# Kernel tuning notes

Hardware: AMD Instinct MI355X
Metric: run time of the kernel (lower is better)

The kernel has to match this reference:

```python
import jax, jax.numpy as jnp
import numpy as np

D_K = 64


def setup_inputs() -> dict:
    key = jax.random.key(0)
    kq, kk, kv, km = jax.random.split(key, 4)
    B, H, S = 4, 16, 2048
    Q = jax.random.normal(kq, (B, H, S, D_K), dtype=jnp.float32)
    K = jax.random.normal(kk, (B, H, S, D_K), dtype=jnp.float32)
    V = jax.random.normal(kv, (B, H, S, D_K), dtype=jnp.float32)
    # boolean mask, True = masked out; broadcast over heads
    mask = jax.random.randint(km, (B, 1, S, S), 0, 2).astype(jnp.bool_)
    return {"Q": Q, "K": K, "V": V, "mask": mask}


def reference(Q, K, V, mask):
    scale = jnp.sqrt(jnp.asarray(D_K, dtype=Q.dtype))
    # [B,H,S,S] scores
    scores = jnp.einsum('bhqd,bhkd->bhqk', Q, K) / scale
    scores = jnp.where(mask, jnp.asarray(-1e9, dtype=scores.dtype), scores)
    attn = jax.nn.softmax(scores, axis=-1)
    return jnp.einsum('bhqk,bhkd->bhqd', attn, V)
```

## Files before the change

kernel.cpp:

```cpp
#include <hip/hip_runtime.h>
#include <hip/hip_bf16.h>


#define SEQ   2048
#define DK    64
#define NB_   4
#define NBH   64
#define KVB   64
#define QB    128

#define MASKH_WORDS ((size_t)NB_ * SEQ * 64)

typedef float    f32x16 __attribute__((ext_vector_type(16)));
typedef _Float16 f16x8  __attribute__((ext_vector_type(8)));

#define QSCALE 0.18033688011112042f
#define MBIAS  (-5.0f)
#define CH     264

#if __has_builtin(__builtin_amdgcn_exp2f)
#define EXP2F(x) __builtin_amdgcn_exp2f(x)
#else
#define EXP2F(x) exp2f(x)
#endif

__device__ __forceinline__ unsigned pkrtz(float lo, float hi) {
  auto v = __builtin_amdgcn_cvt_pkrtz(lo, hi);
  return __builtin_bit_cast(unsigned, v);
}

#define BARRIER()                                          \
  do {                                                     \
    asm volatile("s_waitcnt lgkmcnt(0)" ::: "memory");     \
    __builtin_amdgcn_s_barrier();                          \
  } while (0)

__device__ __forceinline__ void halfswap(unsigned a, unsigned b,
                                         unsigned& out_lo, unsigned& out_hi, int hiL) {
#if __has_builtin(__builtin_amdgcn_permlane32_swap)
  auto r = __builtin_amdgcn_permlane32_swap(a, b, false, false);
  out_lo = r[0];
  out_hi = r[1];
#else
  unsigned ax = __shfl_xor(a, 32), bx = __shfl_xor(b, 32);
  out_lo = hiL ? bx : a;
  out_hi = hiL ? b : ax;
#endif
}

__global__ __launch_bounds__(256) void mask_pack2(const int* __restrict__ M,
                                                  unsigned* __restrict__ P) {
  int t  = blockIdx.x * 256 + threadIdx.x;
  int hi = t & 1, T = (t >> 1) & 31, q = (t >> 6) & 2047, b = t >> 17;
  const int* src = M + ((size_t)b * SEQ + q) * SEQ + T * 64 + 4 * hi;
  unsigned bits = 0;
#pragma unroll
  for (int kvb = 0; kvb < 2; ++kvb)
#pragma unroll
    for (int m = 0; m < 4; ++m) {
      int4 v = *(const int4*)(src + 32 * kvb + 8 * m);
      int sh = 16 * kvb + 4 * m;
      bits |= ((unsigned)(v.x != 0) << sh) | ((unsigned)(v.y != 0) << (sh + 1)) |
              ((unsigned)(v.z != 0) << (sh + 2)) | ((unsigned)(v.w != 0) << (sh + 3));
    }
  P[t] = bits;
}

template <bool PACKED>
__global__ __launch_bounds__(256) void sda_attn_kernel(
    const float* __restrict__ Q, const float* __restrict__ K,
    const float* __restrict__ V, const int* __restrict__ M,
    const unsigned* __restrict__ Mh, float* __restrict__ O) {
  __shared__ __align__(16) _Float16 Kl[16 * CH];
  __shared__ __align__(16) _Float16 Vt[16 * CH];

  const int bh   = blockIdx.x;
  const int qt   = blockIdx.y;
  const int b    = bh >> 4;
  const int tid  = threadIdx.x;
  const int wid  = tid >> 6;
  const int lane = tid & 63;
  const int lq   = lane & 31;
  const int hiL  = lane >> 5;

  const size_t base = (size_t)bh * SEQ * DK;
  const int    q    = qt * QB + wid * 32 + lq;

  f16x8 qf[4];
  {
    const float* qp = Q + base + (size_t)q * DK + hiL * 8;
#pragma unroll
    for (int kk = 0; kk < 4; ++kk) {
      float4 A  = *(const float4*)(qp + kk * 16);
      float4 Bv = *(const float4*)(qp + kk * 16 + 4);
      uint4 u;
      u.x = pkrtz(A.x * QSCALE, A.y * QSCALE);
      u.y = pkrtz(A.z * QSCALE, A.w * QSCALE);
      u.z = pkrtz(Bv.x * QSCALE, Bv.y * QSCALE);
      u.w = pkrtz(Bv.z * QSCALE, Bv.w * QSCALE);
      qf[kk] = __builtin_bit_cast(f16x8, u);
    }
  }

  f32x16 oacc[2];
#pragma unroll
  for (int db = 0; db < 2; ++db)
#pragma unroll
    for (int r = 0; r < 16; ++r) oacc[db][r] = 0.f;
  float lreg = 0.f;

  const int krow = tid >> 2, c0 = tid & 3;
  const int kp   = tid & 31, d8 = (tid >> 5) * 8;
  const float* Kg  = K + base + (size_t)krow * DK + c0 * 16;
  const float* Vg0 = V + base + (size_t)(2 * kp) * DK + d8;
  const float* Vg1 = Vg0 + DK;

  const int kwa = ((krow >> 5) * 8 + c0 * 2) * CH + (krow & 31) * 8;
  const int kwb = kwa + CH;
  const int vwb = ((d8 >> 5) * 8 + (kp >> 3) * 2 + ((kp >> 2) & 1)) * CH +
                  (d8 & 31) * 8 + (kp & 3) * 2;

  float4 kpre[4], vpre[4];
#define LOADT(kb_)                                                        \
  {                                                                       \
    const float* kg = Kg + (size_t)(kb_)*DK;                              \
    _Pragma("unroll") for (int i = 0; i < 4; ++i)                         \
        kpre[i] = *(const float4*)(kg + 4 * i);                           \
    const float* va = Vg0 + (size_t)(kb_)*DK;                             \
    const float* vb = Vg1 + (size_t)(kb_)*DK;                             \
    vpre[0] = *(const float4*)va; vpre[1] = *(const float4*)(va + 4);     \
    vpre[2] = *(const float4*)vb; vpre[3] = *(const float4*)(vb + 4);     \
  }
  LOADT(0);

  const unsigned* Mhp  = PACKED ? Mh + ((size_t)b * SEQ + q) * 64 + hiL : nullptr;
  const int*      Mrow = PACKED ? nullptr : M + ((size_t)b * SEQ + q) * SEQ + 4 * hiL;

  for (int kb = 0; kb < SEQ; kb += KVB) {
    unsigned mw = 0;
    int4 mraw[8];
    if (PACKED) {
      mw = Mhp[kb >> 5];
    } else {
#pragma unroll
      for (int kvb = 0; kvb < 2; ++kvb)
#pragma unroll
        for (int m = 0; m < 4; ++m)
          mraw[kvb * 4 + m] = *(const int4*)(Mrow + kb + 32 * kvb + 8 * m);
    }

    BARRIER();

    {
      uint4 u0, u1;
      u0.x = pkrtz(kpre[0].x, kpre[0].y); u0.y = pkrtz(kpre[0].z, kpre[0].w);
      u0.z = pkrtz(kpre[1].x, kpre[1].y); u0.w = pkrtz(kpre[1].z, kpre[1].w);
      u1.x = pkrtz(kpre[2].x, kpre[2].y); u1.y = pkrtz(kpre[2].z, kpre[2].w);
      u1.z = pkrtz(kpre[3].x, kpre[3].y); u1.w = pkrtz(kpre[3].z, kpre[3].w);
      *(uint4*)&Kl[kwa] = u0;
      *(uint4*)&Kl[kwb] = u1;
      const float* va = (const float*)&vpre[0];
      const float* vc = (const float*)&vpre[2];
#pragma unroll
      for (int j = 0; j < 8; ++j)
        *(unsigned*)&Vt[vwb + j * 8] = pkrtz(va[j], vc[j]);
    }
    BARRIER();

    if (kb + KVB < SEQ) LOADT(kb + KVB);

    f32x16 sc[2];
#pragma unroll
    for (int kvb = 0; kvb < 2; ++kvb)
#pragma unroll
      for (int r = 0; r < 16; ++r) sc[kvb][r] = MBIAS;

    __builtin_amdgcn_s_setprio(1);
#pragma unroll
    for (int kvb = 0; kvb < 2; ++kvb)
#pragma unroll
      for (int kk = 0; kk < 4; ++kk) {
        f16x8 kf = *(const f16x8*)&Kl[(kvb * 8 + kk * 2 + hiL) * CH + lq * 8];
        sc[kvb] = __builtin_amdgcn_mfma_f32_32x32x16_f16(kf, qf[kk], sc[kvb], 0, 0, 0);
      }
    __builtin_amdgcn_s_setprio(0);

    float rs = 0.f;
    unsigned pr[2][4][2];
#pragma unroll
    for (int kvb = 0; kvb < 2; ++kvb) {
      float e[16];
#pragma unroll
      for (int r = 0; r < 16; ++r) {
        float ev = EXP2F(sc[kvb][r]);
        bool msk;
        if (PACKED) {
          msk = ((mw >> (16 * kvb + r)) & 1u) != 0u;
        } else {
          int4 v = mraw[kvb * 4 + (r >> 2)];
          int mm = (r & 3) == 0 ? v.x : (r & 3) == 1 ? v.y : (r & 3) == 2 ? v.z : v.w;
          msk = mm != 0;
        }
        ev = msk ? 0.f : ev;
        e[r] = ev;
        rs += ev;
      }
#pragma unroll
      for (int m = 0; m < 4; ++m) {
        pr[kvb][m][0] = pkrtz(e[4 * m + 0], e[4 * m + 1]);
        pr[kvb][m][1] = pkrtz(e[4 * m + 2], e[4 * m + 3]);
      }
    }

    {
      unsigned ru = __builtin_bit_cast(unsigned, rs), plo, phi;
      halfswap(ru, ru, plo, phi, hiL);
      float other = __builtin_bit_cast(float, hiL ? plo : phi);
      lreg += rs + other;
    }

#pragma unroll
    for (int ks = 0; ks < 4; ++ks) {
      const int kvb = ks >> 1, ms = (ks & 1) * 2;
      unsigned w0, w1, w2, w3;
      halfswap(pr[kvb][ms][0], pr[kvb][ms + 1][0], w0, w2, hiL);
      halfswap(pr[kvb][ms][1], pr[kvb][ms + 1][1], w1, w3, hiL);
      f16x8 pf = __builtin_bit_cast(f16x8, make_uint4(w0, w1, w2, w3));

      __builtin_amdgcn_s_setprio(1);
#pragma unroll
      for (int db = 0; db < 2; ++db) {
        f16x8 vf = *(const f16x8*)&Vt[(db * 8 + ks * 2 + hiL) * CH + lq * 8];
        oacc[db] = __builtin_amdgcn_mfma_f32_32x32x16_f16(vf, pf, oacc[db], 0, 0, 0);
      }
      __builtin_amdgcn_s_setprio(0);
    }
  }

  float inv = (lreg > 0.f) ? 1.0f / lreg : 0.f;
  float* op = O + base + (size_t)q * DK + 4 * hiL;
#pragma unroll
  for (int db = 0; db < 2; ++db)
#pragma unroll
    for (int m = 0; m < 4; ++m) {
      float4 o;
      o.x = oacc[db][4 * m + 0] * inv;
      o.y = oacc[db][4 * m + 1] * inv;
      o.z = oacc[db][4 * m + 2] * inv;
      o.w = oacc[db][4 * m + 3] * inv;
      *(float4*)(op + 32 * db + 8 * m) = o;
    }
}

extern "C" void kernel_launch(void* const* d_in, const int* in_sizes, int n_in,
                              void* d_out, int out_size, void* d_ws, size_t ws_size,
                              hipStream_t stream) {
  const float* Q = (const float*)d_in[0];
  const float* K = (const float*)d_in[1];
  const float* V = (const float*)d_in[2];
  const int*   M = (const int*)d_in[3];
  float*       O = (float*)d_out;
  dim3 grid(NBH, SEQ / QB);

  if (ws_size >= MASKH_WORDS * 4) {
    unsigned* Mh = (unsigned*)d_ws;
    mask_pack2<<<(int)(MASKH_WORDS / 256), 256, 0, stream>>>(M, Mh);
    sda_attn_kernel<true><<<grid, 256, 0, stream>>>(Q, K, V, M, Mh, O);
  } else {
    sda_attn_kernel<false><<<grid, 256, 0, stream>>>(Q, K, V, M, nullptr, O);
  }
}
```

Measured before the change: 159.7 us.

## Double-buffer K/V LDS tiles to overlap staging with compute, one barrier per tile

Splits the K and V shared-memory tiles into two buffers. The next tile is converted and written into the idle buffer right after the QK MFMAs, and the global prefetch moves two tiles ahead. This cuts the loop from two block barriers per KV tile to one and lets LDS writes overlap with softmax and PV work. In exchange it doubles LDS use (about 33 KB per block), which may reduce occupancy, and it keeps more registers live for the deeper prefetch.

```diff
diff --git a/kernel.cpp b/kernel.cpp
--- a/kernel.cpp
+++ b/kernel.cpp
@@ -8,6 +8,7 @@
 #define NBH   64
 #define KVB   64
 #define QB    128
+#define NT    (SEQ / KVB)
 
 #define MASKH_WORDS ((size_t)NB_ * SEQ * 64)
 
@@ -71,8 +72,8 @@
     const float* __restrict__ Q, const float* __restrict__ K,
     const float* __restrict__ V, const int* __restrict__ M,
     const unsigned* __restrict__ Mh, float* __restrict__ O) {
-  __shared__ __align__(16) _Float16 Kl[16 * CH];
-  __shared__ __align__(16) _Float16 Vt[16 * CH];
+  __shared__ __align__(16) _Float16 Kl[2][16 * CH];
+  __shared__ __align__(16) _Float16 Vt[2][16 * CH];
 
   const int bh   = blockIdx.x;
   const int qt   = blockIdx.y;
@@ -131,59 +132,66 @@
     vpre[0] = *(const float4*)va; vpre[1] = *(const float4*)(va + 4);     \
     vpre[2] = *(const float4*)vb; vpre[3] = *(const float4*)(vb + 4);     \
   }
-  LOADT(0);
+
+#define STAGE(b_)                                                         \
+  {                                                                       \
+    uint4 u0, u1;                                                         \
+    u0.x = pkrtz(kpre[0].x, kpre[0].y); u0.y = pkrtz(kpre[0].z, kpre[0].w); \
+    u0.z = pkrtz(kpre[1].x, kpre[1].y); u0.w = pkrtz(kpre[1].z, kpre[1].w); \
+    u1.x = pkrtz(kpre[2].x, kpre[2].y); u1.y = pkrtz(kpre[2].z, kpre[2].w); \
+    u1.z = pkrtz(kpre[3].x, kpre[3].y); u1.w = pkrtz(kpre[3].z, kpre[3].w); \
+    *(uint4*)&Kl[b_][kwa] = u0;                                           \
+    *(uint4*)&Kl[b_][kwb] = u1;                                           \
+    const float* va_ = (const float*)&vpre[0];                            \
+    const float* vc_ = (const float*)&vpre[2];                            \
+    _Pragma("unroll") for (int j = 0; j < 8; ++j)                         \
+        *(unsigned*)&Vt[b_][vwb + j * 8] = pkrtz(va_[j], vc_[j]);         \
+  }
 
   const unsigned* Mhp  = PACKED ? Mh + ((size_t)b * SEQ + q) * 64 + hiL : nullptr;
   const int*      Mrow = PACKED ? nullptr : M + ((size_t)b * SEQ + q) * SEQ + 4 * hiL;
 
-  for (int kb = 0; kb < SEQ; kb += KVB) {
-    unsigned mw = 0;
+  LOADT(0);
+  STAGE(0);
+  LOADT(KVB);
+  unsigned mw_cur = PACKED ? Mhp[0] : 0u;
+  BARRIER();
+
+  for (int t = 0; t < NT; ++t) {
+    const int cur = t & 1;
+
+    f32x16 sc[2];
+#pragma unroll
+    for (int kvb = 0; kvb < 2; ++kvb)
+#pragma unroll
+      for (int r = 0; r < 16; ++r) sc[kvb][r] = MBIAS;
+
+    __builtin_amdgcn_s_setprio(1);
+#pragma unroll
+    for (int kk = 0; kk < 4; ++kk)
+#pragma unroll
+      for (int kvb = 0; kvb < 2; ++kvb) {
+        f16x8 kf = *(const f16x8*)&Kl[cur][(kvb * 8 + kk * 2 + hiL) * CH + lq * 8];
+        sc[kvb] = __builtin_amdgcn_mfma_f32_32x32x16_f16(kf, qf[kk], sc[kvb], 0, 0, 0);
+      }
+    __builtin_amdgcn_s_setprio(0);
+
+    const bool more = (t + 1 < NT);
+    unsigned mw_next = 0;
+    if (more) {
+      STAGE(cur ^ 1);
+      if (t + 2 < NT) LOADT((t + 2) * KVB);
+      if (PACKED) mw_next = Mhp[2 * (t + 1)];
+    }
+
     int4 mraw[8];
-    if (PACKED) {
-      mw = Mhp[kb >> 5];
-    } else {
+    if (!PACKED) {
 #pragma unroll
       for (int kvb = 0; kvb < 2; ++kvb)
 #pragma unroll
         for (int m = 0; m < 4; ++m)
-          mraw[kvb * 4 + m] = *(const int4*)(Mrow + kb + 32 * kvb + 8 * m);
-    }
-
-    BARRIER();
-
-    {
-      uint4 u0, u1;
-      u0.x = pkrtz(kpre[0].x, kpre[0].y); u0.y = pkrtz(kpre[0].z, kpre[0].w);
-      u0.z = pkrtz(kpre[1].x, kpre[1].y); u0.w = pkrtz(kpre[1].z, kpre[1].w);
-      u1.x = pkrtz(kpre[2].x, kpre[2].y); u1.y = pkrtz(kpre[2].z, kpre[2].w);
-      u1.z = pkrtz(kpre[3].x, kpre[3].y); u1.w = pkrtz(kpre[3].z, kpre[3].w);
-      *(uint4*)&Kl[kwa] = u0;
-      *(uint4*)&Kl[kwb] = u1;
-      const float* va = (const float*)&vpre[0];
-      const float* vc = (const float*)&vpre[2];
-#pragma unroll
-      for (int j = 0; j < 8; ++j)
-        *(unsigned*)&Vt[vwb + j * 8] = pkrtz(va[j], vc[j]);
-    }
-    BARRIER();
-
-    if (kb + KVB < SEQ) LOADT(kb + KVB);
-
-    f32x16 sc[2];
-#pragma unroll
-    for (int kvb = 0; kvb < 2; ++kvb)
-#pragma unroll
-      for (int r = 0; r < 16; ++r) sc[kvb][r] = MBIAS;
-
-    __builtin_amdgcn_s_setprio(1);
-#pragma unroll
-    for (int kvb = 0; kvb < 2; ++kvb)
-#pragma unroll
-      for (int kk = 0; kk < 4; ++kk) {
-        f16x8 kf = *(const f16x8*)&Kl[(kvb * 8 + kk * 2 + hiL) * CH + lq * 8];
-        sc[kvb] = __builtin_amdgcn_mfma_f32_32x32x16_f16(kf, qf[kk], sc[kvb], 0, 0, 0);
-      }
-    __builtin_amdgcn_s_setprio(0);
+          mraw[kvb * 4 + m] = *(const int4*)(Mrow + t * KVB + 32 * kvb + 8 * m);
+    }
 
     float rs = 0.f;
     unsigned pr[2][4][2];
@@ -195,7 +203,7 @@
         float ev = EXP2F(sc[kvb][r]);
         bool msk;
         if (PACKED) {
-          msk = ((mw >> (16 * kvb + r)) & 1u) != 0u;
+          msk = ((mw_cur >> (16 * kvb + r)) & 1u) != 0u;
         } else {
           int4 v = mraw[kvb * 4 + (r >> 2)];
           int mm = (r & 3) == 0 ? v.x : (r & 3) == 1 ? v.y : (r & 3) == 2 ? v.z : v.w;
@@ -230,11 +238,14 @@
       __builtin_amdgcn_s_setprio(1);
 #pragma unroll
       for (int db = 0; db < 2; ++db) {
-        f16x8 vf = *(const f16x8*)&Vt[(db * 8 + ks * 2 + hiL) * CH + lq * 8];
+        f16x8 vf = *(const f16x8*)&Vt[cur][(db * 8 + ks * 2 + hiL) * CH + lq * 8];
         oacc[db] = __builtin_amdgcn_mfma_f32_32x32x16_f16(vf, pf, oacc[db], 0, 0, 0);
       }
       __builtin_amdgcn_s_setprio(0);
     }
+
+    mw_cur = mw_next;
+    if (more) BARRIER();
   }
 
   float inv = (lreg > 0.f) ? 1.0f / lreg : 0.f;
```

Measured after the change: 144.9 us. -9.3%, faster.
